# Kernel optimization log

Hardware: AMD Instinct MI355X
Metric: run time of the kernel (lower is better)

## Reference

```python
import jax, jax.numpy as jnp
import numpy as np

HIDDEN = 1024
N_HEAD = 16
HEAD_DIM = HIDDEN // N_HEAD


def setup_inputs() -> dict:
    key = jax.random.key(0)
    ks = jax.random.split(key, 11)
    B, S, D, H, E = 4, 1024, HIDDEN, N_HEAD, HEAD_DIM
    sc = 0.02
    return {
        "query": jax.random.normal(ks[0], (B, S, D), jnp.float32),
        "key": jax.random.normal(ks[1], (B, S, D), jnp.float32),
        "value": jax.random.normal(ks[2], (B, S, D), jnp.float32),
        # per-head projection weights stacked over heads (torch Linear: y = x @ W.T + b)
        "Wq": jax.random.normal(ks[3], (H, D, E), jnp.float32) * sc,
        "bq": jax.random.normal(ks[4], (H, E), jnp.float32) * sc,
        "Wk": jax.random.normal(ks[5], (H, D, E), jnp.float32) * sc,
        "bk": jax.random.normal(ks[6], (H, E), jnp.float32) * sc,
        "Wv": jax.random.normal(ks[7], (H, D, E), jnp.float32) * sc,
        "bv": jax.random.normal(ks[8], (H, E), jnp.float32) * sc,
        "Wo": jax.random.normal(ks[9], (D, D), jnp.float32) * sc,
        "bo": jax.random.normal(ks[10], (D,), jnp.float32) * sc,
    }


def reference(query, key, value, Wq, bq, Wk, bk, Wv, bv, Wo, bo):
    B, S, D = query.shape
    H, _, E = Wq.shape
    # per-head linear projections (vectorized over heads)
    q = jnp.einsum("bsd,hde->bhse", query, Wq) + bq[None, :, None, :]
    k = jnp.einsum("bsd,hde->bhse", key, Wk) + bk[None, :, None, :]
    v = jnp.einsum("bsd,hde->bhse", value, Wv) + bv[None, :, None, :]
    scale = jnp.sqrt(jnp.asarray(E, q.dtype))
    scores = jnp.einsum("bhse,bhte->bhst", q, k) / scale  # [B,H,S,S]
    attn = jax.nn.softmax(scores, axis=-1)  # dropout is identity in eval
    wv = jnp.einsum("bhst,bhte->bhse", attn, v)  # [B,H,S,E]
    # concat heads along feature dim (head h -> slice h*E:(h+1)*E)
    wv = wv.transpose(0, 2, 1, 3).reshape(B, S, H * E)
    out = wv @ Wo.T + bo  # final linear; output dropout identity in eval
    return out
```

## Files before the change

### kernel.cpp

```cpp
#include <hip/hip_runtime.h>

typedef unsigned short u16;
typedef unsigned int u32;
typedef __attribute__((ext_vector_type(8))) short bf16x8;
typedef __attribute__((ext_vector_type(4))) float f32x4;

#define B_SZ 4
#define S_SZ 1024
#define D_SZ 1024
#define H_SZ 16
#define E_SZ 64
#define M_SZ (B_SZ * S_SZ)

__device__ __forceinline__ u16 f2bf(float f) {
  union { float f; unsigned u; } x; x.f = f;
  unsigned r = (x.u + 0x7FFFu + ((x.u >> 16) & 1u)) >> 16;
  return (u16)r;
}

__device__ __forceinline__ u32 pack_bf16(float lo, float hi) {
  return (u32)f2bf(lo) | ((u32)f2bf(hi) << 16);
}

__device__ __forceinline__ void async16(const void* g, void* l) {
  __builtin_amdgcn_global_load_lds(
      (const __attribute__((address_space(1))) void*)g,
      (__attribute__((address_space(3))) void*)l, 16, 0, 0);
}

__device__ __forceinline__ f32x4 mfma16(bf16x8 a, bf16x8 b, f32x4 c) {
  return __builtin_amdgcn_mfma_f32_16x16x32_bf16(a, b, c, 0, 0, 0);
}

__global__ void cast4(const float* __restrict__ q, const float* __restrict__ k,
                      const float* __restrict__ v, const float* __restrict__ Wo,
                      u16* __restrict__ oq, u16* __restrict__ ok,
                      u16* __restrict__ ov, u16* __restrict__ oWo) {
  int gid = blockIdx.x * 256 + threadIdx.x;
  const float* in;
  u16* out;
  int i;
  if (gid < (3 << 19)) {
    int sel = gid >> 19;
    i = (gid & ((1 << 19) - 1)) << 3;
    in = sel == 0 ? q : (sel == 1 ? k : v);
    out = sel == 0 ? oq : (sel == 1 ? ok : ov);
  } else {
    i = (gid - (3 << 19)) << 3;
    in = Wo;
    out = oWo;
  }
  float4 a = *(const float4*)(in + i);
  float4 b = *(const float4*)(in + i + 4);
  alignas(16) u16 r[8];
  r[0] = f2bf(a.x); r[1] = f2bf(a.y); r[2] = f2bf(a.z); r[3] = f2bf(a.w);
  r[4] = f2bf(b.x); r[5] = f2bf(b.y); r[6] = f2bf(b.z); r[7] = f2bf(b.w);
  *(uint4*)(out + i) = *(uint4*)r;
}

__global__ void transW3(const float* __restrict__ Wq, const float* __restrict__ Wk,
                        const float* __restrict__ Wv, u16* __restrict__ Tq,
                        u16* __restrict__ Tk, u16* __restrict__ Tv) {
  __shared__ float tile[64 * 68];
  const int wsel = blockIdx.x >> 8;
  const int bi = blockIdx.x & 255;
  const float* W = wsel == 0 ? Wq : (wsel == 1 ? Wk : Wv);
  u16* WT = wsel == 0 ? Tq : (wsel == 1 ? Tk : Tv);
  const int tid = threadIdx.x;
  const int h = bi >> 4;
  const int d0 = (bi & 15) << 6;
#pragma unroll
  for (int c = 0; c < 4; ++c) {
    const int dd = c * 16 + (tid >> 4);
    const int e4 = (tid & 15) << 2;
    float4 vq = *(const float4*)(W + (h << 16) + ((d0 + dd) << 6) + e4);
    *(float4*)(tile + dd * 68 + e4) = vq;
  }
  __syncthreads();
  {
    const int e = tid >> 2;
    const int dc = (tid & 3) << 4;
    alignas(16) u16 outv[16];
#pragma unroll
    for (int i = 0; i < 16; ++i) outv[i] = f2bf(tile[(dc + i) * 68 + e]);
    u16* dst = WT + (((size_t)(h << 6) + e) << 10) + d0 + dc;
    *(uint4*)(dst) = *(uint4*)outv;
    *(uint4*)(dst + 8) = *(uint4*)(outv + 8);
  }
}

__global__ __launch_bounds__(256)
void gemm3(const u16* __restrict__ qb, const u16* __restrict__ kb, const u16* __restrict__ vb,
           const u16* __restrict__ Tq, const u16* __restrict__ Tk, const u16* __restrict__ Tv,
           const float* __restrict__ bq, const float* __restrict__ bk, const float* __restrict__ bv,
           u16* __restrict__ Qp, u16* __restrict__ Kp, u16* __restrict__ VpT) {
  __shared__ u16 Al[128 * 64];
  __shared__ u16 Bl[128 * 64];
  const int wg = blockIdx.x;
  const int swz = (wg & 7) * 96 + (wg >> 3);
  const int g = swz >> 8;
  const int bi = swz & 255;
  const u16* A = g == 0 ? qb : (g == 1 ? kb : vb);
  const u16* BT = g == 0 ? Tq : (g == 1 ? Tk : Tv);
  const float* bias = g == 0 ? bq : (g == 1 ? bk : bv);
  u16* Cout = g == 0 ? Qp : (g == 1 ? Kp : VpT);
  const float scale = g == 0 ? 0.125f : 1.0f;

  const int tid = threadIdx.x;
  const int wave = tid >> 6;
  const int lane = tid & 63;
  const int l15 = lane & 15, lq = lane >> 4;
  const int bm = bi >> 3;
  const int bn = bi & 7;
  const int row0 = bm << 7, col0 = bn << 7;
  const int wr = ((wave >> 1) & 1) << 6;
  const int wc = (wave & 1) << 6;

  f32x4 acc[4][4];
#pragma unroll
  for (int m = 0; m < 4; ++m)
#pragma unroll
    for (int n = 0; n < 4; ++n) acc[m][n] = (f32x4)0.0f;

  for (int k0 = 0; k0 < 1024; k0 += 64) {
    __syncthreads();
#pragma unroll
    for (int c = 0; c < 4; ++c) {
      const int x = c * 4096 + tid * 16;
      const int gx = x ^ (((x >> 7) & 7) << 4);
      const int row = gx >> 7;
      const int cb = gx & 127;
      const u16* ga = A + (size_t)(row0 + row) * 1024 + k0 + (cb >> 1);
      const u16* gb = BT + (size_t)(col0 + row) * 1024 + k0 + (cb >> 1);
      async16(ga, (char*)Al + x);
      async16(gb, (char*)Bl + x);
    }
    __syncthreads();

    bf16x8 af[4][2], bfr[4][2];
#pragma unroll
    for (int m = 0; m < 4; ++m)
#pragma unroll
      for (int kf = 0; kf < 2; ++kf) {
        int r = wr + m * 16 + l15;
        int byte = ((r << 7) + kf * 64 + lq * 16) ^ ((r & 7) << 4);
        af[m][kf] = *(const bf16x8*)((const char*)Al + byte);
      }
#pragma unroll
    for (int n = 0; n < 4; ++n)
#pragma unroll
      for (int kf = 0; kf < 2; ++kf) {
        int r = wc + n * 16 + l15;
        int byte = ((r << 7) + kf * 64 + lq * 16) ^ ((r & 7) << 4);
        bfr[n][kf] = *(const bf16x8*)((const char*)Bl + byte);
      }
    if (g == 2) {
#pragma unroll
      for (int kf = 0; kf < 2; ++kf)
#pragma unroll
        for (int m = 0; m < 4; ++m)
#pragma unroll
          for (int n = 0; n < 4; ++n)
            acc[m][n] = mfma16(af[m][kf], bfr[n][kf], acc[m][n]);
    } else {
#pragma unroll
      for (int kf = 0; kf < 2; ++kf)
#pragma unroll
        for (int m = 0; m < 4; ++m)
#pragma unroll
          for (int n = 0; n < 4; ++n)
            acc[m][n] = mfma16(bfr[n][kf], af[m][kf], acc[m][n]);
    }
  }

  if (g == 2) {
#pragma unroll
    for (int m = 0; m < 4; ++m)
#pragma unroll
      for (int n = 0; n < 4; ++n) {
        int col = col0 + wc + n * 16 + l15;
        float bv = bias[col];
        int rowb = row0 + wr + m * 16 + lq * 4;
        alignas(8) u16 r4[4];
#pragma unroll
        for (int j = 0; j < 4; ++j) r4[j] = f2bf(acc[m][n][j] + bv);
        *(uint2*)(Cout + (size_t)col * 4096 + rowb) = *(uint2*)r4;
      }
  } else {
    float4 b4[4];
#pragma unroll
    for (int n = 0; n < 4; ++n)
      b4[n] = *(const float4*)(bias + col0 + wc + n * 16 + lq * 4);
#pragma unroll
    for (int m = 0; m < 4; ++m) {
      int row = row0 + wr + m * 16 + l15;
#pragma unroll
      for (int n = 0; n < 4; ++n) {
        int colbase = col0 + wc + n * 16 + lq * 4;
        u32 lo = pack_bf16((acc[m][n][0] + b4[n].x) * scale,
                           (acc[m][n][1] + b4[n].y) * scale);
        u32 hi = pack_bf16((acc[m][n][2] + b4[n].z) * scale,
                           (acc[m][n][3] + b4[n].w) * scale);
        uint2 wv; wv.x = lo; wv.y = hi;
        *(uint2*)(Cout + (size_t)row * 1024 + colbase) = wv;
      }
    }
  }
}

__global__ __launch_bounds__(512, 4)
void gemmO8(const u16* __restrict__ A, const u16* __restrict__ BT,
            const float* __restrict__ bias, float* __restrict__ out) {
  __shared__ u16 Al[2][128 * 64];
  __shared__ u16 Bl[2][128 * 64];
  const int tid = threadIdx.x;
  const int wave = tid >> 6;
  const int lane = tid & 63;
  const int l15 = lane & 15, lq = lane >> 4;
  const int wg = blockIdx.x;
  const int bi = (wg & 7) * 32 + (wg >> 3);
  const int bm = bi >> 3;
  const int bn = bi & 7;
  const int row0 = bm << 7, col0 = bn << 7;
  const int wr = (wave >> 1) << 5;
  const int wc = (wave & 1) << 6;

  int xs[2], rowS[2], cbS[2];
#pragma unroll
  for (int c = 0; c < 2; ++c) {
    int x = c * 8192 + tid * 16;
    int gx = x ^ (((x >> 7) & 7) << 4);
    xs[c] = x;
    rowS[c] = gx >> 7;
    cbS[c] = (gx & 127) >> 1;
  }

  f32x4 acc[2][4];
#pragma unroll
  for (int m = 0; m < 2; ++m)
#pragma unroll
    for (int n = 0; n < 4; ++n) acc[m][n] = (f32x4)0.0f;

#pragma unroll
  for (int c = 0; c < 2; ++c) {
    async16(A + (size_t)(row0 + rowS[c]) * 1024 + cbS[c], (char*)Al[0] + xs[c]);
    async16(BT + (size_t)(col0 + rowS[c]) * 1024 + cbS[c], (char*)Bl[0] + xs[c]);
  }
  __syncthreads();

  int buf = 0;
  for (int k0 = 0; k0 < 1024; k0 += 64) {
    if (k0 + 64 < 1024) {
      const int kn = k0 + 64;
#pragma unroll
      for (int c = 0; c < 2; ++c) {
        async16(A + (size_t)(row0 + rowS[c]) * 1024 + kn + cbS[c], (char*)Al[buf ^ 1] + xs[c]);
        async16(BT + (size_t)(col0 + rowS[c]) * 1024 + kn + cbS[c], (char*)Bl[buf ^ 1] + xs[c]);
      }
    }

    bf16x8 af[2][2], bfr[4][2];
#pragma unroll
    for (int m = 0; m < 2; ++m)
#pragma unroll
      for (int kf = 0; kf < 2; ++kf) {
        int r = wr + m * 16 + l15;
        int byte = ((r << 7) + kf * 64 + lq * 16) ^ ((r & 7) << 4);
        af[m][kf] = *(const bf16x8*)((const char*)Al[buf] + byte);
      }
#pragma unroll
    for (int n = 0; n < 4; ++n)
#pragma unroll
      for (int kf = 0; kf < 2; ++kf) {
        int r = wc + n * 16 + l15;
        int byte = ((r << 7) + kf * 64 + lq * 16) ^ ((r & 7) << 4);
        bfr[n][kf] = *(const bf16x8*)((const char*)Bl[buf] + byte);
      }
#pragma unroll
    for (int kf = 0; kf < 2; ++kf)
#pragma unroll
      for (int m = 0; m < 2; ++m)
#pragma unroll
        for (int n = 0; n < 4; ++n)
          acc[m][n] = mfma16(bfr[n][kf], af[m][kf], acc[m][n]);

    __syncthreads();
    buf ^= 1;
  }

  float4 b4[4];
#pragma unroll
  for (int n = 0; n < 4; ++n)
    b4[n] = *(const float4*)(bias + col0 + wc + n * 16 + lq * 4);
#pragma unroll
  for (int m = 0; m < 2; ++m) {
    int row = row0 + wr + m * 16 + l15;
#pragma unroll
    for (int n = 0; n < 4; ++n) {
      int colbase = col0 + wc + n * 16 + lq * 4;
      float4 v;
      v.x = acc[m][n][0] + b4[n].x;
      v.y = acc[m][n][1] + b4[n].y;
      v.z = acc[m][n][2] + b4[n].z;
      v.w = acc[m][n][3] + b4[n].w;
      *(float4*)(out + (size_t)row * 1024 + colbase) = v;
    }
  }
}

__global__ __launch_bounds__(256)
void attn(const u16* __restrict__ Qp, const u16* __restrict__ Kp,
          const u16* __restrict__ VpT, u16* __restrict__ Ow) {
  __shared__ alignas(16) u16 Kl[2][64 * 64];
  __shared__ alignas(16) u16 VTl[2][64 * 64];
  __shared__ alignas(16) u16 Pl[4][2][16 * 64];
  const int tid = threadIdx.x;
  const int wave = tid >> 6;
  const int lane = tid & 63;
  const int l15 = lane & 15, lq = lane >> 4;
  const int wg = blockIdx.x;
  const int swz = (wg & 7) * 64 + (wg >> 3);
  const int qt = swz & 7;
  const int bh = swz >> 3;
  const int b = bh >> 4, h = bh & 15;
  const size_t bS = (size_t)b * S_SZ;

  const int xs0 = tid * 16, xs1 = 4096 + tid * 16;
  const int r0 = xs0 >> 7, r1 = xs1 >> 7;
  const int c0 = ((xs0 & 127) ^ (((xs0 >> 7) & 7) << 4)) >> 1;
  const int c1 = ((xs1 & 127) ^ (((xs1 >> 7) & 7) << 4)) >> 1;
  const u16* Kb0 = Kp + ((bS + r0) << 10) + h * 64 + c0;
  const u16* Kb1 = Kp + ((bS + r1) << 10) + h * 64 + c1;
  const u16* Vb0 = VpT + (size_t)(h * 64 + r0) * 4096 + bS + c0;
  const u16* Vb1 = VpT + (size_t)(h * 64 + r1) * 4096 + bS + c1;

  bf16x8 aq0[2], aq1[2];
  {
    const u16* qp0 = Qp + ((bS + qt * 128 + wave * 32 + l15) << 10) + h * 64 + lq * 8;
    aq0[0] = *(const bf16x8*)(qp0);
    aq0[1] = *(const bf16x8*)(qp0 + 32);
    const u16* qp1 = qp0 + (16 << 10);
    aq1[0] = *(const bf16x8*)(qp1);
    aq1[1] = *(const bf16x8*)(qp1 + 32);
  }

  f32x4 o0[4], o1[4];
#pragma unroll
  for (int n = 0; n < 4; ++n) { o0[n] = (f32x4)0.0f; o1[n] = (f32x4)0.0f; }
  float m0 = -1e30f, m1 = -1e30f;
  float l0 = 0.f, l1 = 0.f;
  u16* Pw0 = Pl[wave][0];
  u16* Pw1 = Pl[wave][1];

  async16(Kb0, (char*)Kl[0] + xs0);
  async16(Kb1, (char*)Kl[0] + xs1);
  async16(Vb0, (char*)VTl[0] + xs0);
  async16(Vb1, (char*)VTl[0] + xs1);
  __syncthreads();

  int buf = 0;
  for (int t0 = 0; t0 < S_SZ; t0 += 64) {
    if (t0 + 64 < S_SZ) {
      const int tn = t0 + 64;
      async16(Kb0 + ((size_t)tn << 10), (char*)Kl[buf ^ 1] + xs0);
      async16(Kb1 + ((size_t)tn << 10), (char*)Kl[buf ^ 1] + xs1);
      async16(Vb0 + tn, (char*)VTl[buf ^ 1] + xs0);
      async16(Vb1 + tn, (char*)VTl[buf ^ 1] + xs1);
    }

    f32x4 s0[4], s1[4];
#pragma unroll
    for (int n = 0; n < 4; ++n) { s0[n] = (f32x4)0.0f; s1[n] = (f32x4)0.0f; }
    __builtin_amdgcn_s_setprio(1);
#pragma unroll
    for (int n = 0; n < 4; ++n)
#pragma unroll
      for (int kf = 0; kf < 2; ++kf) {
        int r = n * 16 + l15;
        int byte = ((r << 7) + kf * 64 + lq * 16) ^ ((r & 7) << 4);
        bf16x8 bk = *(const bf16x8*)((const char*)Kl[buf] + byte);
        s0[n] = mfma16(bk, aq0[kf], s0[n]);
        s1[n] = mfma16(bk, aq1[kf], s1[n]);
      }
    __builtin_amdgcn_s_setprio(0);

    {
      float mx = s0[0][0];
#pragma unroll
      for (int n = 0; n < 4; ++n)
#pragma unroll
        for (int j = 0; j < 4; ++j) mx = fmaxf(mx, s0[n][j]);
      mx = fmaxf(mx, __shfl_xor(mx, 16, 64));
      mx = fmaxf(mx, __shfl_xor(mx, 32, 64));
      if (__any(mx > m0 + 8.0f)) {
        float mn = fmaxf(m0, mx);
        float alpha = __expf(m0 - mn);
        m0 = mn;
        l0 *= alpha;
        float a0 = __shfl(alpha, lq * 4 + 0, 64);
        float a1 = __shfl(alpha, lq * 4 + 1, 64);
        float a2 = __shfl(alpha, lq * 4 + 2, 64);
        float a3 = __shfl(alpha, lq * 4 + 3, 64);
#pragma unroll
        for (int n = 0; n < 4; ++n) {
          o0[n][0] *= a0; o0[n][1] *= a1; o0[n][2] *= a2; o0[n][3] *= a3;
        }
      }
      float rs = 0.f;
#pragma unroll
      for (int n = 0; n < 4; ++n) {
        float p0 = __expf(s0[n][0] - m0);
        float p1 = __expf(s0[n][1] - m0);
        float p2 = __expf(s0[n][2] - m0);
        float p3 = __expf(s0[n][3] - m0);
        rs += (p0 + p1) + (p2 + p3);
        u32 lo = pack_bf16(p0, p1);
        u32 hi = pack_bf16(p2, p3);
        int byte = (l15 << 7) + (((n * 32 + lq * 8)) ^ ((l15 & 7) << 4));
        uint2 wv; wv.x = lo; wv.y = hi;
        *(uint2*)((char*)Pw0 + byte) = wv;
      }
      rs += __shfl_xor(rs, 16, 64);
      rs += __shfl_xor(rs, 32, 64);
      l0 += rs;
    }
    {
      float mx = s1[0][0];
#pragma unroll
      for (int n = 0; n < 4; ++n)
#pragma unroll
        for (int j = 0; j < 4; ++j) mx = fmaxf(mx, s1[n][j]);
      mx = fmaxf(mx, __shfl_xor(mx, 16, 64));
      mx = fmaxf(mx, __shfl_xor(mx, 32, 64));
      if (__any(mx > m1 + 8.0f)) {
        float mn = fmaxf(m1, mx);
        float alpha = __expf(m1 - mn);
        m1 = mn;
        l1 *= alpha;
        float a0 = __shfl(alpha, lq * 4 + 0, 64);
        float a1 = __shfl(alpha, lq * 4 + 1, 64);
        float a2 = __shfl(alpha, lq * 4 + 2, 64);
        float a3 = __shfl(alpha, lq * 4 + 3, 64);
#pragma unroll
        for (int n = 0; n < 4; ++n) {
          o1[n][0] *= a0; o1[n][1] *= a1; o1[n][2] *= a2; o1[n][3] *= a3;
        }
      }
      float rs = 0.f;
#pragma unroll
      for (int n = 0; n < 4; ++n) {
        float p0 = __expf(s1[n][0] - m1);
        float p1 = __expf(s1[n][1] - m1);
        float p2 = __expf(s1[n][2] - m1);
        float p3 = __expf(s1[n][3] - m1);
        rs += (p0 + p1) + (p2 + p3);
        u32 lo = pack_bf16(p0, p1);
        u32 hi = pack_bf16(p2, p3);
        int byte = (l15 << 7) + (((n * 32 + lq * 8)) ^ ((l15 & 7) << 4));
        uint2 wv; wv.x = lo; wv.y = hi;
        *(uint2*)((char*)Pw1 + byte) = wv;
      }
      rs += __shfl_xor(rs, 16, 64);
      rs += __shfl_xor(rs, 32, 64);
      l1 += rs;
    }

    __builtin_amdgcn_s_setprio(1);
#pragma unroll
    for (int kf = 0; kf < 2; ++kf) {
      int pbyte = (l15 << 7) + ((kf * 64 + lq * 16) ^ ((l15 & 7) << 4));
      bf16x8 pa0 = *(const bf16x8*)((const char*)Pw0 + pbyte);
      bf16x8 pa1 = *(const bf16x8*)((const char*)Pw1 + pbyte);
#pragma unroll
      for (int n = 0; n < 4; ++n) {
        int vr = n * 16 + l15;
        int byte = ((vr << 7) + kf * 64 + lq * 16) ^ ((vr & 7) << 4);
        bf16x8 bv = *(const bf16x8*)((const char*)VTl[buf] + byte);
        o0[n] = mfma16(pa0, bv, o0[n]);
        o1[n] = mfma16(pa1, bv, o1[n]);
      }
    }
    __builtin_amdgcn_s_setprio(0);

    __syncthreads();
    buf ^= 1;
  }

#pragma unroll
  for (int qg = 0; qg < 2; ++qg) {
    float lr = qg == 0 ? l0 : l1;
    f32x4* o = qg == 0 ? o0 : o1;
    float li0 = __shfl(lr, lq * 4 + 0, 64);
    float li1 = __shfl(lr, lq * 4 + 1, 64);
    float li2 = __shfl(lr, lq * 4 + 2, 64);
    float li3 = __shfl(lr, lq * 4 + 3, 64);
    float inv0 = 1.0f / li0, inv1 = 1.0f / li1, inv2 = 1.0f / li2, inv3 = 1.0f / li3;
#pragma unroll
    for (int n = 0; n < 4; ++n) {
      float vals[4] = {o[n][0] * inv0, o[n][1] * inv1, o[n][2] * inv2, o[n][3] * inv3};
#pragma unroll
      for (int j = 0; j < 4; ++j) {
        int row = qt * 128 + wave * 32 + qg * 16 + lq * 4 + j;
        int col = h * 64 + n * 16 + l15;
        Ow[((bS + row) << 10) + col] = f2bf(vals[j]);
      }
    }
  }
}

extern "C" void kernel_launch(void* const* d_in, const int* in_sizes, int n_in,
                              void* d_out, int out_size, void* d_ws, size_t ws_size,
                              hipStream_t stream) {
  const float* q  = (const float*)d_in[0];
  const float* k  = (const float*)d_in[1];
  const float* v  = (const float*)d_in[2];
  const float* Wq = (const float*)d_in[3];
  const float* bq = (const float*)d_in[4];
  const float* Wk = (const float*)d_in[5];
  const float* bk = (const float*)d_in[6];
  const float* Wv = (const float*)d_in[7];
  const float* bv = (const float*)d_in[8];
  const float* Wo = (const float*)d_in[9];
  const float* bo = (const float*)d_in[10];

  char* w = (char*)d_ws;
  const size_t MB = 1u << 20;
  u16* qb  = (u16*)(w + 0 * MB);
  u16* kb  = (u16*)(w + 8 * MB);
  u16* vb  = (u16*)(w + 16 * MB);
  u16* WqT = (u16*)(w + 24 * MB);
  u16* WkT = (u16*)(w + 26 * MB);
  u16* WvT = (u16*)(w + 28 * MB);
  u16* Wob = (u16*)(w + 30 * MB);
  u16* Qp  = (u16*)(w + 32 * MB);
  u16* Kp  = (u16*)(w + 40 * MB);
  u16* VpT = (u16*)(w + 48 * MB);
  u16* wvb = (u16*)(w + 56 * MB);

  cast4<<<6656, 256, 0, stream>>>(q, k, v, Wo, qb, kb, vb, Wob);
  transW3<<<768, 256, 0, stream>>>(Wq, Wk, Wv, WqT, WkT, WvT);

  gemm3<<<768, 256, 0, stream>>>(qb, kb, vb, WqT, WkT, WvT, bq, bk, bv, Qp, Kp, VpT);

  attn<<<512, 256, 0, stream>>>(Qp, Kp, VpT, wvb);

  gemmO8<<<256, 512, 0, stream>>>(wvb, Wob, bo, (float*)d_out);
}
```

Baseline: 121.7 us.

## Fuse fp32-to-bf16 input casts into projection GEMMs and double-buffer gemm3

Removes the separate cast kernel. The QKV projection GEMM and the output GEMM now read fp32 activations and Wo directly through registers, convert them to bf16, and store them to LDS themselves. gemm3 also gains double-buffered LDS, with the next tile's loads issued before the MFMA work. This drops one kernel launch and a round trip of bf16 copies through memory. In exchange, the A tile in gemm3 reads twice the bytes from global memory, and each of the 8 column blocks rereads it. It also adds register pressure and LDS usage (double buffers) that may lower occupancy.

Measured after the change: 169.3 us. 39.1% more time.

```diff
diff --git a/kernel.cpp b/kernel.cpp
--- a/kernel.cpp
+++ b/kernel.cpp
@@ -30,32 +30,6 @@
 
 __device__ __forceinline__ f32x4 mfma16(bf16x8 a, bf16x8 b, f32x4 c) {
   return __builtin_amdgcn_mfma_f32_16x16x32_bf16(a, b, c, 0, 0, 0);
-}
-
-__global__ void cast4(const float* __restrict__ q, const float* __restrict__ k,
-                      const float* __restrict__ v, const float* __restrict__ Wo,
-                      u16* __restrict__ oq, u16* __restrict__ ok,
-                      u16* __restrict__ ov, u16* __restrict__ oWo) {
-  int gid = blockIdx.x * 256 + threadIdx.x;
-  const float* in;
-  u16* out;
-  int i;
-  if (gid < (3 << 19)) {
-    int sel = gid >> 19;
-    i = (gid & ((1 << 19) - 1)) << 3;
-    in = sel == 0 ? q : (sel == 1 ? k : v);
-    out = sel == 0 ? oq : (sel == 1 ? ok : ov);
-  } else {
-    i = (gid - (3 << 19)) << 3;
-    in = Wo;
-    out = oWo;
-  }
-  float4 a = *(const float4*)(in + i);
-  float4 b = *(const float4*)(in + i + 4);
-  alignas(16) u16 r[8];
-  r[0] = f2bf(a.x); r[1] = f2bf(a.y); r[2] = f2bf(a.z); r[3] = f2bf(a.w);
-  r[4] = f2bf(b.x); r[5] = f2bf(b.y); r[6] = f2bf(b.z); r[7] = f2bf(b.w);
-  *(uint4*)(out + i) = *(uint4*)r;
 }
 
 __global__ void transW3(const float* __restrict__ Wq, const float* __restrict__ Wk,
@@ -90,17 +64,18 @@
 }
 
 __global__ __launch_bounds__(256)
-void gemm3(const u16* __restrict__ qb, const u16* __restrict__ kb, const u16* __restrict__ vb,
+void gemm3(const float* __restrict__ qf, const float* __restrict__ kf,
+           const float* __restrict__ vf,
            const u16* __restrict__ Tq, const u16* __restrict__ Tk, const u16* __restrict__ Tv,
            const float* __restrict__ bq, const float* __restrict__ bk, const float* __restrict__ bv,
            u16* __restrict__ Qp, u16* __restrict__ Kp, u16* __restrict__ VpT) {
-  __shared__ u16 Al[128 * 64];
-  __shared__ u16 Bl[128 * 64];
+  __shared__ u16 Al[2][128 * 64];
+  __shared__ u16 Bl[2][128 * 64];
   const int wg = blockIdx.x;
   const int swz = (wg & 7) * 96 + (wg >> 3);
   const int g = swz >> 8;
   const int bi = swz & 255;
-  const u16* A = g == 0 ? qb : (g == 1 ? kb : vb);
+  const float* A32 = g == 0 ? qf : (g == 1 ? kf : vf);
   const u16* BT = g == 0 ? Tq : (g == 1 ? Tk : Tv);
   const float* bias = g == 0 ? bq : (g == 1 ? bk : bv);
   u16* Cout = g == 0 ? Qp : (g == 1 ? Kp : VpT);
@@ -116,61 +91,105 @@
   const int wr = ((wave >> 1) & 1) << 6;
   const int wc = (wave & 1) << 6;
 
+  int xs[4];
+  const float* Af[4];
+  const u16* Bb[4];
+#pragma unroll
+  for (int c = 0; c < 4; ++c) {
+    int x = c * 4096 + tid * 16;
+    int gx = x ^ (((x >> 7) & 7) << 4);
+    int rowS = gx >> 7;
+    int cbS = (gx & 127) >> 1;
+    xs[c] = x;
+    Af[c] = A32 + (size_t)(row0 + rowS) * 1024 + cbS;
+    Bb[c] = BT + (size_t)(col0 + rowS) * 1024 + cbS;
+  }
+
   f32x4 acc[4][4];
 #pragma unroll
   for (int m = 0; m < 4; ++m)
 #pragma unroll
     for (int n = 0; n < 4; ++n) acc[m][n] = (f32x4)0.0f;
 
+  float4 pf[4][2];
+#pragma unroll
+  for (int c = 0; c < 4; ++c) {
+    pf[c][0] = *(const float4*)(Af[c]);
+    pf[c][1] = *(const float4*)(Af[c] + 4);
+    async16(Bb[c], (char*)Bl[0] + xs[c]);
+  }
+#pragma unroll
+  for (int c = 0; c < 4; ++c) {
+    uint4 wv;
+    wv.x = pack_bf16(pf[c][0].x, pf[c][0].y);
+    wv.y = pack_bf16(pf[c][0].z, pf[c][0].w);
+    wv.z = pack_bf16(pf[c][1].x, pf[c][1].y);
+    wv.w = pack_bf16(pf[c][1].z, pf[c][1].w);
+    *(uint4*)((char*)Al[0] + xs[c]) = wv;
+  }
+  __syncthreads();
+
+  int buf = 0;
   for (int k0 = 0; k0 < 1024; k0 += 64) {
+    const bool nxt = (k0 + 64 < 1024);
+    if (nxt) {
+      const int kn = k0 + 64;
+#pragma unroll
+      for (int c = 0; c < 4; ++c) {
+        pf[c][0] = *(const float4*)(Af[c] + kn);
+        pf[c][1] = *(const float4*)(Af[c] + kn + 4);
+        async16(Bb[c] + kn, (char*)Bl[buf ^ 1] + xs[c]);
+      }
+    }
+
+    bf16x8 af[4][2], bfr[4][2];
+#pragma unroll
+    for (int m = 0; m < 4; ++m)
+#pragma unroll
+      for (int kf2 = 0; kf2 < 2; ++kf2) {
+        int r = wr + m * 16 + l15;
+        int byte = ((r << 7) + kf2 * 64 + lq * 16) ^ ((r & 7) << 4);
+        af[m][kf2] = *(const bf16x8*)((const char*)Al[buf] + byte);
+      }
+#pragma unroll
+    for (int n = 0; n < 4; ++n)
+#pragma unroll
+      for (int kf2 = 0; kf2 < 2; ++kf2) {
+        int r = wc + n * 16 + l15;
+        int byte = ((r << 7) + kf2 * 64 + lq * 16) ^ ((r & 7) << 4);
+        bfr[n][kf2] = *(const bf16x8*)((const char*)Bl[buf] + byte);
+      }
+    if (g == 2) {
+#pragma unroll
+      for (int kf2 = 0; kf2 < 2; ++kf2)
+#pragma unroll
+        for (int m = 0; m < 4; ++m)
+#pragma unroll
+          for (int n = 0; n < 4; ++n)
+            acc[m][n] = mfma16(af[m][kf2], bfr[n][kf2], acc[m][n]);
+    } else {
+#pragma unroll
+      for (int kf2 = 0; kf2 < 2; ++kf2)
+#pragma unroll
+        for (int m = 0; m < 4; ++m)
+#pragma unroll
+          for (int n = 0; n < 4; ++n)
+            acc[m][n] = mfma16(bfr[n][kf2], af[m][kf2], acc[m][n]);
+    }
+
+    if (nxt) {
+#pragma unroll
+      for (int c = 0; c < 4; ++c) {
+        uint4 wv;
+        wv.x = pack_bf16(pf[c][0].x, pf[c][0].y);
+        wv.y = pack_bf16(pf[c][0].z, pf[c][0].w);
+        wv.z = pack_bf16(pf[c][1].x, pf[c][1].y);
+        wv.w = pack_bf16(pf[c][1].z, pf[c][1].w);
+        *(uint4*)((char*)Al[buf ^ 1] + xs[c]) = wv;
+      }
+    }
     __syncthreads();
-#pragma unroll
-    for (int c = 0; c < 4; ++c) {
-      const int x = c * 4096 + tid * 16;
-      const int gx = x ^ (((x >> 7) & 7) << 4);
-      const int row = gx >> 7;
-      const int cb = gx & 127;
-      const u16* ga = A + (size_t)(row0 + row) * 1024 + k0 + (cb >> 1);
-      const u16* gb = BT + (size_t)(col0 + row) * 1024 + k0 + (cb >> 1);
-      async16(ga, (char*)Al + x);
-      async16(gb, (char*)Bl + x);
-    }
-    __syncthreads();
-
-    bf16x8 af[4][2], bfr[4][2];
-#pragma unroll
-    for (int m = 0; m < 4; ++m)
-#pragma unroll
-      for (int kf = 0; kf < 2; ++kf) {
-        int r = wr + m * 16 + l15;
-        int byte = ((r << 7) + kf * 64 + lq * 16) ^ ((r & 7) << 4);
-        af[m][kf] = *(const bf16x8*)((const char*)Al + byte);
-      }
-#pragma unroll
-    for (int n = 0; n < 4; ++n)
-#pragma unroll
-      for (int kf = 0; kf < 2; ++kf) {
-        int r = wc + n * 16 + l15;
-        int byte = ((r << 7) + kf * 64 + lq * 16) ^ ((r & 7) << 4);
-        bfr[n][kf] = *(const bf16x8*)((const char*)Bl + byte);
-      }
-    if (g == 2) {
-#pragma unroll
-      for (int kf = 0; kf < 2; ++kf)
-#pragma unroll
-        for (int m = 0; m < 4; ++m)
-#pragma unroll
-          for (int n = 0; n < 4; ++n)
-            acc[m][n] = mfma16(af[m][kf], bfr[n][kf], acc[m][n]);
-    } else {
-#pragma unroll
-      for (int kf = 0; kf < 2; ++kf)
-#pragma unroll
-        for (int m = 0; m < 4; ++m)
-#pragma unroll
-          for (int n = 0; n < 4; ++n)
-            acc[m][n] = mfma16(bfr[n][kf], af[m][kf], acc[m][n]);
-    }
+    buf ^= 1;
   }
 
   if (g == 2) {
@@ -209,7 +228,7 @@
 }
 
 __global__ __launch_bounds__(512, 4)
-void gemmO8(const u16* __restrict__ A, const u16* __restrict__ BT,
+void gemmO8(const u16* __restrict__ A, const float* __restrict__ Wo32,
             const float* __restrict__ bias, float* __restrict__ out) {
   __shared__ u16 Al[2][128 * 64];
   __shared__ u16 Bl[2][128 * 64];
@@ -225,14 +244,18 @@
   const int wr = (wave >> 1) << 5;
   const int wc = (wave & 1) << 6;
 
-  int xs[2], rowS[2], cbS[2];
+  int xs[2];
+  const u16* Ab[2];
+  const float* Bf[2];
 #pragma unroll
   for (int c = 0; c < 2; ++c) {
     int x = c * 8192 + tid * 16;
     int gx = x ^ (((x >> 7) & 7) << 4);
+    int rowS = gx >> 7;
+    int cbS = (gx & 127) >> 1;
     xs[c] = x;
-    rowS[c] = gx >> 7;
-    cbS[c] = (gx & 127) >> 1;
+    Ab[c] = A + (size_t)(row0 + rowS) * 1024 + cbS;
+    Bf[c] = Wo32 + (size_t)(col0 + rowS) * 1024 + cbS;
   }
 
   f32x4 acc[2][4];
@@ -241,21 +264,34 @@
 #pragma unroll
     for (int n = 0; n < 4; ++n) acc[m][n] = (f32x4)0.0f;
 
+  float4 pf[2][2];
 #pragma unroll
   for (int c = 0; c < 2; ++c) {
-    async16(A + (size_t)(row0 + rowS[c]) * 1024 + cbS[c], (char*)Al[0] + xs[c]);
-    async16(BT + (size_t)(col0 + rowS[c]) * 1024 + cbS[c], (char*)Bl[0] + xs[c]);
+    async16(Ab[c], (char*)Al[0] + xs[c]);
+    pf[c][0] = *(const float4*)(Bf[c]);
+    pf[c][1] = *(const float4*)(Bf[c] + 4);
+  }
+#pragma unroll
+  for (int c = 0; c < 2; ++c) {
+    uint4 wv;
+    wv.x = pack_bf16(pf[c][0].x, pf[c][0].y);
+    wv.y = pack_bf16(pf[c][0].z, pf[c][0].w);
+    wv.z = pack_bf16(pf[c][1].x, pf[c][1].y);
+    wv.w = pack_bf16(pf[c][1].z, pf[c][1].w);
+    *(uint4*)((char*)Bl[0] + xs[c]) = wv;
   }
   __syncthreads();
 
   int buf = 0;
   for (int k0 = 0; k0 < 1024; k0 += 64) {
-    if (k0 + 64 < 1024) {
+    const bool nxt = (k0 + 64 < 1024);
+    if (nxt) {
       const int kn = k0 + 64;
 #pragma unroll
       for (int c = 0; c < 2; ++c) {
-        async16(A + (size_t)(row0 + rowS[c]) * 1024 + kn + cbS[c], (char*)Al[buf ^ 1] + xs[c]);
-        async16(BT + (size_t)(col0 + rowS[c]) * 1024 + kn + cbS[c], (char*)Bl[buf ^ 1] + xs[c]);
+        async16(Ab[c] + kn, (char*)Al[buf ^ 1] + xs[c]);
+        pf[c][0] = *(const float4*)(Bf[c] + kn);
+        pf[c][1] = *(const float4*)(Bf[c] + kn + 4);
       }
     }
 
@@ -263,27 +299,38 @@
 #pragma unroll
     for (int m = 0; m < 2; ++m)
 #pragma unroll
-      for (int kf = 0; kf < 2; ++kf) {
+      for (int kf2 = 0; kf2 < 2; ++kf2) {
         int r = wr + m * 16 + l15;
-        int byte = ((r << 7) + kf * 64 + lq * 16) ^ ((r & 7) << 4);
-        af[m][kf] = *(const bf16x8*)((const char*)Al[buf] + byte);
+        int byte = ((r << 7) + kf2 * 64 + lq * 16) ^ ((r & 7) << 4);
+        af[m][kf2] = *(const bf16x8*)((const char*)Al[buf] + byte);
       }
 #pragma unroll
     for (int n = 0; n < 4; ++n)
 #pragma unroll
-      for (int kf = 0; kf < 2; ++kf) {
+      for (int kf2 = 0; kf2 < 2; ++kf2) {
         int r = wc + n * 16 + l15;
-        int byte = ((r << 7) + kf * 64 + lq * 16) ^ ((r & 7) << 4);
-        bfr[n][kf] = *(const bf16x8*)((const char*)Bl[buf] + byte);
-      }
-#pragma unroll
-    for (int kf = 0; kf < 2; ++kf)
+        int byte = ((r << 7) + kf2 * 64 + lq * 16) ^ ((r & 7) << 4);
+        bfr[n][kf2] = *(const bf16x8*)((const char*)Bl[buf] + byte);
+      }
+#pragma unroll
+    for (int kf2 = 0; kf2 < 2; ++kf2)
 #pragma unroll
       for (int m = 0; m < 2; ++m)
 #pragma unroll
         for (int n = 0; n < 4; ++n)
-          acc[m][n] = mfma16(bfr[n][kf], af[m][kf], acc[m][n]);
-
+          acc[m][n] = mfma16(bfr[n][kf2], af[m][kf2], acc[m][n]);
+
+    if (nxt) {
+#pragma unroll
+      for (int c = 0; c < 2; ++c) {
+        uint4 wv;
+        wv.x = pack_bf16(pf[c][0].x, pf[c][0].y);
+        wv.y = pack_bf16(pf[c][0].z, pf[c][0].w);
+        wv.z = pack_bf16(pf[c][1].x, pf[c][1].y);
+        wv.w = pack_bf16(pf[c][1].z, pf[c][1].w);
+        *(uint4*)((char*)Bl[buf ^ 1] + xs[c]) = wv;
+      }
+    }
     __syncthreads();
     buf ^= 1;
   }
@@ -375,12 +422,12 @@
 #pragma unroll
     for (int n = 0; n < 4; ++n)
 #pragma unroll
-      for (int kf = 0; kf < 2; ++kf) {
+      for (int kf2 = 0; kf2 < 2; ++kf2) {
         int r = n * 16 + l15;
-        int byte = ((r << 7) + kf * 64 + lq * 16) ^ ((r & 7) << 4);
+        int byte = ((r << 7) + kf2 * 64 + lq * 16) ^ ((r & 7) << 4);
         bf16x8 bk = *(const bf16x8*)((const char*)Kl[buf] + byte);
-        s0[n] = mfma16(bk, aq0[kf], s0[n]);
-        s1[n] = mfma16(bk, aq1[kf], s1[n]);
+        s0[n] = mfma16(bk, aq0[kf2], s0[n]);
+        s1[n] = mfma16(bk, aq1[kf2], s1[n]);
       }
     __builtin_amdgcn_s_setprio(0);
 
@@ -467,14 +514,14 @@
 
     __builtin_amdgcn_s_setprio(1);
 #pragma unroll
-    for (int kf = 0; kf < 2; ++kf) {
-      int pbyte = (l15 << 7) + ((kf * 64 + lq * 16) ^ ((l15 & 7) << 4));
+    for (int kf2 = 0; kf2 < 2; ++kf2) {
+      int pbyte = (l15 << 7) + ((kf2 * 64 + lq * 16) ^ ((l15 & 7) << 4));
       bf16x8 pa0 = *(const bf16x8*)((const char*)Pw0 + pbyte);
       bf16x8 pa1 = *(const bf16x8*)((const char*)Pw1 + pbyte);
 #pragma unroll
       for (int n = 0; n < 4; ++n) {
         int vr = n * 16 + l15;
-        int byte = ((vr << 7) + kf * 64 + lq * 16) ^ ((vr & 7) << 4);
+        int byte = ((vr << 7) + kf2 * 64 + lq * 16) ^ ((vr & 7) << 4);
         bf16x8 bv = *(const bf16x8*)((const char*)VTl[buf] + byte);
         o0[n] = mfma16(pa0, bv, o0[n]);
         o1[n] = mfma16(pa1, bv, o1[n]);
@@ -525,24 +572,19 @@
 
   char* w = (char*)d_ws;
   const size_t MB = 1u << 20;
-  u16* qb  = (u16*)(w + 0 * MB);
-  u16* kb  = (u16*)(w + 8 * MB);
-  u16* vb  = (u16*)(w + 16 * MB);
   u16* WqT = (u16*)(w + 24 * MB);
   u16* WkT = (u16*)(w + 26 * MB);
   u16* WvT = (u16*)(w + 28 * MB);
-  u16* Wob = (u16*)(w + 30 * MB);
   u16* Qp  = (u16*)(w + 32 * MB);
   u16* Kp  = (u16*)(w + 40 * MB);
   u16* VpT = (u16*)(w + 48 * MB);
   u16* wvb = (u16*)(w + 56 * MB);
 
-  cast4<<<6656, 256, 0, stream>>>(q, k, v, Wo, qb, kb, vb, Wob);
   transW3<<<768, 256, 0, stream>>>(Wq, Wk, Wv, WqT, WkT, WvT);
 
-  gemm3<<<768, 256, 0, stream>>>(qb, kb, vb, WqT, WkT, WvT, bq, bk, bv, Qp, Kp, VpT);
+  gemm3<<<768, 256, 0, stream>>>(q, k, v, WqT, WkT, WvT, bq, bk, bv, Qp, Kp, VpT);
 
   attn<<<512, 256, 0, stream>>>(Qp, Kp, VpT, wvb);
 
-  gemmO8<<<256, 512, 0, stream>>>(wvb, Wob, bo, (float*)d_out);
-}
+  gemmO8<<<256, 512, 0, stream>>>(wvb, Wo, bo, (float*)d_out);
+}
```

## Fuse fp32-to-bf16 input casts into projection and output GEMM tile loads

Applied to the files above, without the earlier changes.

Removes the separate cast kernel that converted q/k/v and Wo to bf16. The GEMMs now load fp32 tiles directly into LDS and convert them to bf16 while building MFMA fragments. This drops one launch and the bf16 write and re-read round trip. In exchange the GEMMs fetch twice the bytes for the A (or B) operand per k-step and use more LDS, which can lower occupancy in gemmO8, and every tile that reuses the data repeats the conversion.

New measurement: 143.6 us. +18.0%, slower.

```diff
diff --git a/kernel.cpp b/kernel.cpp
--- a/kernel.cpp
+++ b/kernel.cpp
@@ -32,30 +32,16 @@
   return __builtin_amdgcn_mfma_f32_16x16x32_bf16(a, b, c, 0, 0, 0);
 }
 
-__global__ void cast4(const float* __restrict__ q, const float* __restrict__ k,
-                      const float* __restrict__ v, const float* __restrict__ Wo,
-                      u16* __restrict__ oq, u16* __restrict__ ok,
-                      u16* __restrict__ ov, u16* __restrict__ oWo) {
-  int gid = blockIdx.x * 256 + threadIdx.x;
-  const float* in;
-  u16* out;
-  int i;
-  if (gid < (3 << 19)) {
-    int sel = gid >> 19;
-    i = (gid & ((1 << 19) - 1)) << 3;
-    in = sel == 0 ? q : (sel == 1 ? k : v);
-    out = sel == 0 ? oq : (sel == 1 ? ok : ov);
-  } else {
-    i = (gid - (3 << 19)) << 3;
-    in = Wo;
-    out = oWo;
-  }
-  float4 a = *(const float4*)(in + i);
-  float4 b = *(const float4*)(in + i + 4);
-  alignas(16) u16 r[8];
-  r[0] = f2bf(a.x); r[1] = f2bf(a.y); r[2] = f2bf(a.z); r[3] = f2bf(a.w);
-  r[4] = f2bf(b.x); r[5] = f2bf(b.y); r[6] = f2bf(b.z); r[7] = f2bf(b.w);
-  *(uint4*)(out + i) = *(uint4*)r;
+__device__ __forceinline__ bf16x8 frag_from_f32(const char* lds, int r, int cbytes) {
+  int y0 = (r << 8) + (cbytes ^ ((r & 7) << 4));
+  f32x4 v0 = *(const f32x4*)(lds + y0);
+  f32x4 v1 = *(const f32x4*)(lds + (y0 ^ 16));
+  union { u32 u[4]; bf16x8 v; } cv;
+  cv.u[0] = pack_bf16(v0[0], v0[1]);
+  cv.u[1] = pack_bf16(v0[2], v0[3]);
+  cv.u[2] = pack_bf16(v1[0], v1[1]);
+  cv.u[3] = pack_bf16(v1[2], v1[3]);
+  return cv.v;
 }
 
 __global__ void transW3(const float* __restrict__ Wq, const float* __restrict__ Wk,
@@ -90,17 +76,18 @@
 }
 
 __global__ __launch_bounds__(256)
-void gemm3(const u16* __restrict__ qb, const u16* __restrict__ kb, const u16* __restrict__ vb,
+void gemm3(const float* __restrict__ qf, const float* __restrict__ kf,
+           const float* __restrict__ vf,
            const u16* __restrict__ Tq, const u16* __restrict__ Tk, const u16* __restrict__ Tv,
            const float* __restrict__ bq, const float* __restrict__ bk, const float* __restrict__ bv,
            u16* __restrict__ Qp, u16* __restrict__ Kp, u16* __restrict__ VpT) {
-  __shared__ u16 Al[128 * 64];
+  __shared__ float Alf[128 * 64];
   __shared__ u16 Bl[128 * 64];
   const int wg = blockIdx.x;
   const int swz = (wg & 7) * 96 + (wg >> 3);
   const int g = swz >> 8;
   const int bi = swz & 255;
-  const u16* A = g == 0 ? qb : (g == 1 ? kb : vb);
+  const float* A32 = g == 0 ? qf : (g == 1 ? kf : vf);
   const u16* BT = g == 0 ? Tq : (g == 1 ? Tk : Tv);
   const float* bias = g == 0 ? bq : (g == 1 ? bk : bv);
   u16* Cout = g == 0 ? Qp : (g == 1 ? Kp : VpT);
@@ -116,6 +103,25 @@
   const int wr = ((wave >> 1) & 1) << 6;
   const int wc = (wave & 1) << 6;
 
+  int xa[8];
+  const float* Asrc[8];
+#pragma unroll
+  for (int c = 0; c < 8; ++c) {
+    int x = c * 4096 + tid * 16;
+    int gx = x ^ (((x >> 8) & 7) << 4);
+    xa[c] = x;
+    Asrc[c] = A32 + (size_t)(row0 + (gx >> 8)) * 1024 + ((gx & 255) >> 2);
+  }
+  int xb[4];
+  const u16* Bsrc[4];
+#pragma unroll
+  for (int c = 0; c < 4; ++c) {
+    int x = c * 4096 + tid * 16;
+    int gx = x ^ (((x >> 7) & 7) << 4);
+    xb[c] = x;
+    Bsrc[c] = BT + (size_t)(col0 + (gx >> 7)) * 1024 + ((gx & 127) >> 1);
+  }
+
   f32x4 acc[4][4];
 #pragma unroll
   for (int m = 0; m < 4; ++m)
@@ -125,51 +131,42 @@
   for (int k0 = 0; k0 < 1024; k0 += 64) {
     __syncthreads();
 #pragma unroll
-    for (int c = 0; c < 4; ++c) {
-      const int x = c * 4096 + tid * 16;
-      const int gx = x ^ (((x >> 7) & 7) << 4);
-      const int row = gx >> 7;
-      const int cb = gx & 127;
-      const u16* ga = A + (size_t)(row0 + row) * 1024 + k0 + (cb >> 1);
-      const u16* gb = BT + (size_t)(col0 + row) * 1024 + k0 + (cb >> 1);
-      async16(ga, (char*)Al + x);
-      async16(gb, (char*)Bl + x);
-    }
+    for (int c = 0; c < 8; ++c) async16(Asrc[c] + k0, (char*)Alf + xa[c]);
+#pragma unroll
+    for (int c = 0; c < 4; ++c) async16(Bsrc[c] + k0, (char*)Bl + xb[c]);
     __syncthreads();
 
     bf16x8 af[4][2], bfr[4][2];
 #pragma unroll
     for (int m = 0; m < 4; ++m)
 #pragma unroll
-      for (int kf = 0; kf < 2; ++kf) {
-        int r = wr + m * 16 + l15;
-        int byte = ((r << 7) + kf * 64 + lq * 16) ^ ((r & 7) << 4);
-        af[m][kf] = *(const bf16x8*)((const char*)Al + byte);
-      }
+      for (int kk = 0; kk < 2; ++kk)
+        af[m][kk] = frag_from_f32((const char*)Alf, wr + m * 16 + l15,
+                                  kk * 128 + lq * 32);
 #pragma unroll
     for (int n = 0; n < 4; ++n)
 #pragma unroll
-      for (int kf = 0; kf < 2; ++kf) {
+      for (int kk = 0; kk < 2; ++kk) {
         int r = wc + n * 16 + l15;
-        int byte = ((r << 7) + kf * 64 + lq * 16) ^ ((r & 7) << 4);
-        bfr[n][kf] = *(const bf16x8*)((const char*)Bl + byte);
+        int byte = ((r << 7) + kk * 64 + lq * 16) ^ ((r & 7) << 4);
+        bfr[n][kk] = *(const bf16x8*)((const char*)Bl + byte);
       }
     if (g == 2) {
 #pragma unroll
-      for (int kf = 0; kf < 2; ++kf)
+      for (int kk = 0; kk < 2; ++kk)
 #pragma unroll
         for (int m = 0; m < 4; ++m)
 #pragma unroll
           for (int n = 0; n < 4; ++n)
-            acc[m][n] = mfma16(af[m][kf], bfr[n][kf], acc[m][n]);
+            acc[m][n] = mfma16(af[m][kk], bfr[n][kk], acc[m][n]);
     } else {
 #pragma unroll
-      for (int kf = 0; kf < 2; ++kf)
+      for (int kk = 0; kk < 2; ++kk)
 #pragma unroll
         for (int m = 0; m < 4; ++m)
 #pragma unroll
           for (int n = 0; n < 4; ++n)
-            acc[m][n] = mfma16(bfr[n][kf], af[m][kf], acc[m][n]);
+            acc[m][n] = mfma16(bfr[n][kk], af[m][kk], acc[m][n]);
     }
   }
 
@@ -209,10 +206,10 @@
 }
 
 __global__ __launch_bounds__(512, 4)
-void gemmO8(const u16* __restrict__ A, const u16* __restrict__ BT,
+void gemmO8(const u16* __restrict__ A, const float* __restrict__ Wo32,
             const float* __restrict__ bias, float* __restrict__ out) {
   __shared__ u16 Al[2][128 * 64];
-  __shared__ u16 Bl[2][128 * 64];
+  __shared__ float Blf[2][128 * 64];
   const int tid = threadIdx.x;
   const int wave = tid >> 6;
   const int lane = tid & 63;
@@ -225,14 +222,23 @@
   const int wr = (wave >> 1) << 5;
   const int wc = (wave & 1) << 6;
 
-  int xs[2], rowS[2], cbS[2];
+  int xa[2];
+  const u16* Asrc[2];
 #pragma unroll
   for (int c = 0; c < 2; ++c) {
     int x = c * 8192 + tid * 16;
     int gx = x ^ (((x >> 7) & 7) << 4);
-    xs[c] = x;
-    rowS[c] = gx >> 7;
-    cbS[c] = (gx & 127) >> 1;
+    xa[c] = x;
+    Asrc[c] = A + (size_t)(row0 + (gx >> 7)) * 1024 + ((gx & 127) >> 1);
+  }
+  int xbv[4];
+  const float* Bsrc[4];
+#pragma unroll
+  for (int c = 0; c < 4; ++c) {
+    int x = c * 8192 + tid * 16;
+    int gx = x ^ (((x >> 8) & 7) << 4);
+    xbv[c] = x;
+    Bsrc[c] = Wo32 + (size_t)(col0 + (gx >> 8)) * 1024 + ((gx & 255) >> 2);
   }
 
   f32x4 acc[2][4];
@@ -242,10 +248,9 @@
     for (int n = 0; n < 4; ++n) acc[m][n] = (f32x4)0.0f;
 
 #pragma unroll
-  for (int c = 0; c < 2; ++c) {
-    async16(A + (size_t)(row0 + rowS[c]) * 1024 + cbS[c], (char*)Al[0] + xs[c]);
-    async16(BT + (size_t)(col0 + rowS[c]) * 1024 + cbS[c], (char*)Bl[0] + xs[c]);
-  }
+  for (int c = 0; c < 2; ++c) async16(Asrc[c], (char*)Al[0] + xa[c]);
+#pragma unroll
+  for (int c = 0; c < 4; ++c) async16(Bsrc[c], (char*)Blf[0] + xbv[c]);
   __syncthreads();
 
   int buf = 0;
@@ -253,36 +258,33 @@
     if (k0 + 64 < 1024) {
       const int kn = k0 + 64;
 #pragma unroll
-      for (int c = 0; c < 2; ++c) {
-        async16(A + (size_t)(row0 + rowS[c]) * 1024 + kn + cbS[c], (char*)Al[buf ^ 1] + xs[c]);
-        async16(BT + (size_t)(col0 + rowS[c]) * 1024 + kn + cbS[c], (char*)Bl[buf ^ 1] + xs[c]);
-      }
+      for (int c = 0; c < 2; ++c) async16(Asrc[c] + kn, (char*)Al[buf ^ 1] + xa[c]);
+#pragma unroll
+      for (int c = 0; c < 4; ++c) async16(Bsrc[c] + kn, (char*)Blf[buf ^ 1] + xbv[c]);
     }
 
     bf16x8 af[2][2], bfr[4][2];
 #pragma unroll
     for (int m = 0; m < 2; ++m)
 #pragma unroll
-      for (int kf = 0; kf < 2; ++kf) {
+      for (int kk = 0; kk < 2; ++kk) {
         int r = wr + m * 16 + l15;
-        int byte = ((r << 7) + kf * 64 + lq * 16) ^ ((r & 7) << 4);
-        af[m][kf] = *(const bf16x8*)((const char*)Al[buf] + byte);
+        int byte = ((r << 7) + kk * 64 + lq * 16) ^ ((r & 7) << 4);
+        af[m][kk] = *(const bf16x8*)((const char*)Al[buf] + byte);
       }
 #pragma unroll
     for (int n = 0; n < 4; ++n)
 #pragma unroll
-      for (int kf = 0; kf < 2; ++kf) {
-        int r = wc + n * 16 + l15;
-        int byte = ((r << 7) + kf * 64 + lq * 16) ^ ((r & 7) << 4);
-        bfr[n][kf] = *(const bf16x8*)((const char*)Bl[buf] + byte);
-      }
-#pragma unroll
-    for (int kf = 0; kf < 2; ++kf)
+      for (int kk = 0; kk < 2; ++kk)
+        bfr[n][kk] = frag_from_f32((const char*)Blf[buf], wc + n * 16 + l15,
+                                   kk * 128 + lq * 32);
+#pragma unroll
+    for (int kk = 0; kk < 2; ++kk)
 #pragma unroll
       for (int m = 0; m < 2; ++m)
 #pragma unroll
         for (int n = 0; n < 4; ++n)
-          acc[m][n] = mfma16(bfr[n][kf], af[m][kf], acc[m][n]);
+          acc[m][n] = mfma16(bfr[n][kk], af[m][kk], acc[m][n]);
 
     __syncthreads();
     buf ^= 1;
@@ -375,12 +377,12 @@
 #pragma unroll
     for (int n = 0; n < 4; ++n)
 #pragma unroll
-      for (int kf = 0; kf < 2; ++kf) {
+      for (int kk = 0; kk < 2; ++kk) {
         int r = n * 16 + l15;
-        int byte = ((r << 7) + kf * 64 + lq * 16) ^ ((r & 7) << 4);
+        int byte = ((r << 7) + kk * 64 + lq * 16) ^ ((r & 7) << 4);
         bf16x8 bk = *(const bf16x8*)((const char*)Kl[buf] + byte);
-        s0[n] = mfma16(bk, aq0[kf], s0[n]);
-        s1[n] = mfma16(bk, aq1[kf], s1[n]);
+        s0[n] = mfma16(bk, aq0[kk], s0[n]);
+        s1[n] = mfma16(bk, aq1[kk], s1[n]);
       }
     __builtin_amdgcn_s_setprio(0);
 
@@ -467,14 +469,14 @@
 
     __builtin_amdgcn_s_setprio(1);
 #pragma unroll
-    for (int kf = 0; kf < 2; ++kf) {
-      int pbyte = (l15 << 7) + ((kf * 64 + lq * 16) ^ ((l15 & 7) << 4));
+    for (int kk = 0; kk < 2; ++kk) {
+      int pbyte = (l15 << 7) + ((kk * 64 + lq * 16) ^ ((l15 & 7) << 4));
       bf16x8 pa0 = *(const bf16x8*)((const char*)Pw0 + pbyte);
       bf16x8 pa1 = *(const bf16x8*)((const char*)Pw1 + pbyte);
 #pragma unroll
       for (int n = 0; n < 4; ++n) {
         int vr = n * 16 + l15;
-        int byte = ((vr << 7) + kf * 64 + lq * 16) ^ ((vr & 7) << 4);
+        int byte = ((vr << 7) + kk * 64 + lq * 16) ^ ((vr & 7) << 4);
         bf16x8 bv = *(const bf16x8*)((const char*)VTl[buf] + byte);
         o0[n] = mfma16(pa0, bv, o0[n]);
         o1[n] = mfma16(pa1, bv, o1[n]);
@@ -525,24 +527,19 @@
 
   char* w = (char*)d_ws;
   const size_t MB = 1u << 20;
-  u16* qb  = (u16*)(w + 0 * MB);
-  u16* kb  = (u16*)(w + 8 * MB);
-  u16* vb  = (u16*)(w + 16 * MB);
   u16* WqT = (u16*)(w + 24 * MB);
   u16* WkT = (u16*)(w + 26 * MB);
   u16* WvT = (u16*)(w + 28 * MB);
-  u16* Wob = (u16*)(w + 30 * MB);
   u16* Qp  = (u16*)(w + 32 * MB);
   u16* Kp  = (u16*)(w + 40 * MB);
   u16* VpT = (u16*)(w + 48 * MB);
   u16* wvb = (u16*)(w + 56 * MB);
 
-  cast4<<<6656, 256, 0, stream>>>(q, k, v, Wo, qb, kb, vb, Wob);
   transW3<<<768, 256, 0, stream>>>(Wq, Wk, Wv, WqT, WkT, WvT);
 
-  gemm3<<<768, 256, 0, stream>>>(qb, kb, vb, WqT, WkT, WvT, bq, bk, bv, Qp, Kp, VpT);
+  gemm3<<<768, 256, 0, stream>>>(q, k, v, WqT, WkT, WvT, bq, bk, bv, Qp, Kp, VpT);
 
   attn<<<512, 256, 0, stream>>>(Qp, Kp, VpT, wvb);
 
-  gemmO8<<<256, 512, 0, stream>>>(wvb, Wob, bo, (float*)d_out);
-}
+  gemmO8<<<256, 512, 0, stream>>>(wvb, Wo, bo, (float*)d_out);
+}
```
